# Kernel optimization log

Measured on AMD Instinct MI355X. Metric: run time of the kernel, lower is better.

The kernel has to match this reference:

```python
import jax, jax.numpy as jnp
import numpy as np
import math

H = 8        # n_heads
FACTOR = 5   # ProbSparse factor


def layer_norm(x, g, b, eps=1e-5):
    m = x.mean(-1, keepdims=True)
    v = ((x - m) ** 2).mean(-1, keepdims=True)
    return (x - m) / jnp.sqrt(v + eps) * g + b


def conv1d_circular(x, w, b=None):
    # x: [B, L, Cin], w: [Cout, Cin, 3]; Conv1d(k=3, padding=1, padding_mode='circular')
    xp = jnp.concatenate([x[:, -1:], x, x[:, :1]], axis=1)
    y = jax.lax.conv_general_dilated(xp.transpose(0, 2, 1), w, (1,), 'VALID',
                                     dimension_numbers=('NCH', 'OIH', 'NCH'))
    if b is not None:
        y = y + b[None, :, None]
    return y.transpose(0, 2, 1)


def pos_encoding(L, d):
    pos = jnp.arange(L, dtype=jnp.float32)[:, None]
    div = jnp.exp(jnp.arange(0, d, 2, dtype=jnp.float32) * (-math.log(10000.0) / d))
    pe = jnp.zeros((L, d), dtype=jnp.float32)
    pe = pe.at[:, 0::2].set(jnp.sin(pos * div))
    pe = pe.at[:, 1::2].set(jnp.cos(pos * div))
    return pe


def prob_attention(rng, Q, K, V):
    # Q, K, V: [B, H, L, E]; non-causal ProbSparse self-attention (mask_flag=False)
    B, Hh, L, E = Q.shape
    c = FACTOR * int(np.ceil(np.log(L)))
    U_part = min(c, L)  # sampled keys per query (sparsity measurement)
    u = min(c, L)       # number of active (top) queries
    idx = jax.random.randint(rng, (L, U_part), 0, L)          # shared over B,H as in torch
    K_sample = K[:, :, idx]                                   # [B,H,L,U,E] gather
    QK_sample = jnp.einsum('bhle,bhlue->bhlu', Q, K_sample)
    M = QK_sample.max(-1) - QK_sample.sum(-1) / L             # sparsity score per query
    M_top = jax.lax.top_k(M, u)[1]                            # [B,H,u] active query ids
    Q_red = jnp.take_along_axis(Q, M_top[..., None], axis=2)  # [B,H,u,E]
    scores = jnp.einsum('bhue,bhle->bhul', Q_red, K) * (1.0 / math.sqrt(E))
    attn = jax.nn.softmax(scores, axis=-1)
    upd = jnp.einsum('bhul,bhle->bhue', attn, V)
    # initial context: mean of V for every query; overwrite active queries
    ctx = jnp.broadcast_to(V.mean(axis=2, keepdims=True), (B, Hh, L, E))
    bi = jnp.arange(B)[:, None, None]
    hi = jnp.arange(Hh)[None, :, None]
    ctx = ctx.at[bi, hi, M_top].set(upd)
    return ctx.transpose(0, 2, 1, 3)  # [B,L,H,E]


def encoder_layer(rng, x, Wq, bq, Wk, bk, Wv, bv, Wo, bo, g1, b1, w1, bf1, w2, bf2, g2, b2):
    B, L, D = x.shape
    dh = D // H
    q = (x @ Wq.T + bq).reshape(B, L, H, dh).transpose(0, 2, 1, 3)
    k = (x @ Wk.T + bk).reshape(B, L, H, dh).transpose(0, 2, 1, 3)
    v = (x @ Wv.T + bv).reshape(B, L, H, dh).transpose(0, 2, 1, 3)
    o = prob_attention(rng, q, k, v).reshape(B, L, D)
    x = x + (o @ Wo.T + bo)            # dropout is identity in eval
    x = layer_norm(x, g1, b1)
    y = jax.nn.gelu(x @ w1.T + bf1, approximate=False)  # conv1 k=1 == linear
    y = y @ w2.T + bf2
    return layer_norm(x + y, g2, b2)


def conv_distill(x, w, b, bg, bb):
    # Conv1d(circular,k=3) -> BatchNorm1d(eval: mean 0, var 1) -> ELU -> MaxPool1d(3,2,1)
    y = conv1d_circular(x, w, b)
    y = y / math.sqrt(1.0 + 1e-5) * bg + bb
    y = jax.nn.elu(y)
    yc = jnp.pad(y.transpose(0, 2, 1), ((0, 0), (0, 0), (1, 1)), constant_values=-jnp.inf)
    p = jax.lax.reduce_window(yc, -jnp.inf, jax.lax.max, (1, 1, 3), (1, 1, 2), 'VALID')
    return p.transpose(0, 2, 1)  # [B, L//2, D]


def forward(x_enc, emb_w, Wq, bq, Wk, bk, Wv, bv, Wo, bo, ln1_g, ln1_b, ff_w1, ff_b1, ff_w2, ff_b2, ln2_g, ln2_b, cv_w, cv_b, bn_g, bn_b, norm_g, norm_b):
    B, L, _ = x_enc.shape
    D = emb_w.shape[0]
    x = conv1d_circular(x_enc, emb_w) + pos_encoding(L, D)[None]  # GazeEmbedding
    base = jax.random.key(42)
    EL = Wq.shape[0]
    for i in range(EL):
        rng = jax.random.fold_in(base, i)
        x = encoder_layer(rng, x, Wq[i], bq[i], Wk[i], bk[i], Wv[i], bv[i], Wo[i], bo[i],
                          ln1_g[i], ln1_b[i], ff_w1[i], ff_b1[i], ff_w2[i], ff_b2[i], ln2_g[i], ln2_b[i])
        if i < EL - 1:
            x = conv_distill(x, cv_w[i], cv_b[i], bn_g[i], bn_b[i])
    return layer_norm(x, norm_g, norm_b)


def setup_inputs() -> dict:
    key = jax.random.key(0)
    ks = jax.random.split(key, 16)
    B, L, C, D, F, EL = 4, 2048, 2, 512, 512, 3
    s = 0.02
    return {
        'x_enc': jax.random.normal(ks[0], (B, L, C), jnp.float32),
        'emb_w': jax.random.normal(ks[1], (D, C, 3), jnp.float32) * s,
        'Wq': jax.random.normal(ks[2], (EL, D, D), jnp.float32) * s,
        'bq': jnp.zeros((EL, D), jnp.float32),
        'Wk': jax.random.normal(ks[3], (EL, D, D), jnp.float32) * s,
        'bk': jnp.zeros((EL, D), jnp.float32),
        'Wv': jax.random.normal(ks[4], (EL, D, D), jnp.float32) * s,
        'bv': jnp.zeros((EL, D), jnp.float32),
        'Wo': jax.random.normal(ks[5], (EL, D, D), jnp.float32) * s,
        'bo': jnp.zeros((EL, D), jnp.float32),
        'ln1_g': jnp.ones((EL, D), jnp.float32),
        'ln1_b': jnp.zeros((EL, D), jnp.float32),
        'ff_w1': jax.random.normal(ks[6], (EL, F, D), jnp.float32) * s,
        'ff_b1': jnp.zeros((EL, F), jnp.float32),
        'ff_w2': jax.random.normal(ks[7], (EL, D, F), jnp.float32) * s,
        'ff_b2': jnp.zeros((EL, D), jnp.float32),
        'ln2_g': jnp.ones((EL, D), jnp.float32),
        'ln2_b': jnp.zeros((EL, D), jnp.float32),
        'cv_w': jax.random.normal(ks[8], (EL - 1, D, D, 3), jnp.float32) * s,
        'cv_b': jnp.zeros((EL - 1, D), jnp.float32),
        'bn_g': jnp.ones((EL - 1, D), jnp.float32),
        'bn_b': jnp.zeros((EL - 1, D), jnp.float32),
        'norm_g': jnp.ones((D,), jnp.float32),
        'norm_b': jnp.zeros((D,), jnp.float32),
    }


def reference(x_enc, emb_w, Wq, bq, Wk, bk, Wv, bv, Wo, bo, ln1_g, ln1_b, ff_w1, ff_b1, ff_w2, ff_b2, ln2_g, ln2_b, cv_w, cv_b, bn_g, bn_b, norm_g, norm_b):
    return forward(x_enc, emb_w, Wq, bq, Wk, bk, Wv, bv, Wo, bo, ln1_g, ln1_b, ff_w1, ff_b1, ff_w2, ff_b2, ln2_g, ln2_b, cv_w, cv_b, bn_g, bn_b, norm_g, norm_b)
```

## Files before the change

### kernel.cpp

```cpp
#include <hip/hip_runtime.h>
#include <cmath>
#include <cstdint>

#define D_MODEL 512
#define NH 8
#define DH 64

static inline int ceil_div(int a, int b) { return (a + b - 1) / b; }

typedef __attribute__((ext_vector_type(8))) short short8;
typedef __attribute__((ext_vector_type(4))) float floatx4;

__device__ __forceinline__ unsigned short f2bf(float f) {
  uint32_t u = __float_as_uint(f);
  uint32_t r = (u + 0x7fffu + ((u >> 16) & 1u)) >> 16;
  return (unsigned short)r;
}
__device__ __forceinline__ float bf2f(unsigned short s) {
  return __uint_as_float(((uint32_t)s) << 16);
}

#define TF_ROTL(x, r) (((x) << (r)) | ((x) >> (32 - (r))))

__host__ __device__ inline void threefry2x32(uint32_t k0, uint32_t k1,
                                             uint32_t x0, uint32_t x1,
                                             uint32_t* o0, uint32_t* o1) {
  uint32_t ks2 = k0 ^ k1 ^ 0x1BD11BDAu;
  x0 += k0; x1 += k1;
#define TF_R4(a, b, c, d)                                    \
  x0 += x1; x1 = TF_ROTL(x1, a); x1 ^= x0;                   \
  x0 += x1; x1 = TF_ROTL(x1, b); x1 ^= x0;                   \
  x0 += x1; x1 = TF_ROTL(x1, c); x1 ^= x0;                   \
  x0 += x1; x1 = TF_ROTL(x1, d); x1 ^= x0;
  TF_R4(13, 15, 26, 6);  x0 += k1;  x1 += ks2 + 1u;
  TF_R4(17, 29, 16, 24); x0 += ks2; x1 += k0 + 2u;
  TF_R4(13, 15, 26, 6);  x0 += k0;  x1 += k1 + 3u;
  TF_R4(17, 29, 16, 24); x0 += k1;  x1 += ks2 + 4u;
  TF_R4(13, 15, 26, 6);  x0 += ks2; x1 += k0 + 5u;
#undef TF_R4
  *o0 = x0; *o1 = x1;
}

__global__ __launch_bounds__(256) void cast3_qkv_kernel(
    const float* __restrict__ s0, const float* __restrict__ s1,
    const float* __restrict__ s2, unsigned short* __restrict__ dst) {
  int sel = blockIdx.x / 768, bb = blockIdx.x % 768;
  int i = (bb * 256 + threadIdx.x) * 4;
  const float* s = (sel == 0) ? s0 : (sel == 1) ? s1 : s2;
  float4 v = *(const float4*)(s + i);
  ushort4 o;
  o.x = f2bf(v.x); o.y = f2bf(v.y); o.z = f2bf(v.z); o.w = f2bf(v.w);
  int layer = i >> 18, off = i & 262143;
  *(ushort4*)(dst + (size_t)layer * 786432 + sel * 262144 + off) = o;
}

__global__ __launch_bounds__(256) void cast3_flat_kernel(
    const float* __restrict__ s0, const float* __restrict__ s1,
    const float* __restrict__ s2, unsigned short* __restrict__ dst) {
  int sel = blockIdx.x / 768, bb = blockIdx.x % 768;
  int i = (bb * 256 + threadIdx.x) * 4;
  const float* s = (sel == 0) ? s0 : (sel == 1) ? s1 : s2;
  float4 v = *(const float4*)(s + i);
  ushort4 o;
  o.x = f2bf(v.x); o.y = f2bf(v.y); o.z = f2bf(v.z); o.w = f2bf(v.w);
  *(ushort4*)(dst + (size_t)sel * 786432 + i) = o;
}

__global__ __launch_bounds__(256) void cast_cvperm_kernel(
    const float* __restrict__ src, unsigned short* __restrict__ dst) {
  int o = blockIdx.x * 256 + threadIdx.x;
  int m = o / 786432, rem = o % 786432;
  int n = rem / 1536, q = rem % 1536;
  int k = q >> 9, c = q & 511;
  dst[o] = f2bf(src[(size_t)m * 786432 + n * 1536 + c * 3 + k]);
}

__global__ __launch_bounds__(256) void embed_kernel(
    const float* __restrict__ x_enc, const float* __restrict__ emb_w,
    float* __restrict__ x, unsigned short* __restrict__ xb, int B, int L) {
  int i = blockIdx.x * 256 + threadIdx.x;
  int total = B * L * D_MODEL;
  if (i >= total) return;
  int d = i % D_MODEL;
  int l = (i / D_MODEL) % L;
  int b = i / (D_MODEL * L);
  int lm = (l == 0) ? (L - 1) : (l - 1);
  int lp = (l == L - 1) ? 0 : (l + 1);
  const float* w = emb_w + d * 6;
  const float* xb_in = x_enc + (size_t)b * L * 2;
  float acc = 0.f;
  acc += xb_in[lm * 2 + 0] * w[0] + xb_in[l * 2 + 0] * w[1] + xb_in[lp * 2 + 0] * w[2];
  acc += xb_in[lm * 2 + 1] * w[3] + xb_in[l * 2 + 1] * w[4] + xb_in[lp * 2 + 1] * w[5];
  int j = d >> 1;
  const float coef = -0.017988946039015985f;
  float div = expf((float)(2 * j) * coef);
  float ang = (float)l * div;
  float pe = (d & 1) ? cosf(ang) : sinf(ang);
  float v = acc + pe;
  x[i] = v;
  xb[i] = f2bf(v);
}

__global__ __launch_bounds__(256) void ln_kernel(
    const float* __restrict__ in, const float* __restrict__ g,
    const float* __restrict__ b, float* __restrict__ out) {
  int row = blockIdx.x;
  int t = threadIdx.x;
  const float* xr = in + (size_t)row * D_MODEL;
  float v0 = xr[t], v1 = xr[t + 256];
  __shared__ float red[256];
  red[t] = v0 + v1;
  __syncthreads();
  for (int s = 128; s > 0; s >>= 1) { if (t < s) red[t] += red[t + s]; __syncthreads(); }
  float mean = red[0] * (1.0f / 512.0f);
  __syncthreads();
  float d0 = v0 - mean, d1 = v1 - mean;
  red[t] = d0 * d0 + d1 * d1;
  __syncthreads();
  for (int s = 128; s > 0; s >>= 1) { if (t < s) red[t] += red[t + s]; __syncthreads(); }
  float var = red[0] * (1.0f / 512.0f);
  float rstd = 1.0f / sqrtf(var + 1e-5f);
  float* outr = out + (size_t)row * D_MODEL;
  outr[t]       = d0 * rstd * g[t]       + b[t];
  outr[t + 256] = d1 * rstd * g[t + 256] + b[t + 256];
}

__global__ __launch_bounds__(256) void ln_dual_kernel(
    const float* __restrict__ in, const float* __restrict__ g,
    const float* __restrict__ b, float* __restrict__ out,
    unsigned short* __restrict__ out16) {
  int row = blockIdx.x;
  int t = threadIdx.x;
  const float* xr = in + (size_t)row * D_MODEL;
  float v0 = xr[t], v1 = xr[t + 256];
  __shared__ float red[256];
  red[t] = v0 + v1;
  __syncthreads();
  for (int s = 128; s > 0; s >>= 1) { if (t < s) red[t] += red[t + s]; __syncthreads(); }
  float mean = red[0] * (1.0f / 512.0f);
  __syncthreads();
  float d0 = v0 - mean, d1 = v1 - mean;
  red[t] = d0 * d0 + d1 * d1;
  __syncthreads();
  for (int s = 128; s > 0; s >>= 1) { if (t < s) red[t] += red[t + s]; __syncthreads(); }
  float var = red[0] * (1.0f / 512.0f);
  float rstd = 1.0f / sqrtf(var + 1e-5f);
  float* outr = out + (size_t)row * D_MODEL;
  unsigned short* o16 = out16 + (size_t)row * D_MODEL;
  float r0 = d0 * rstd * g[t] + b[t];
  float r1 = d1 * rstd * g[t + 256] + b[t + 256];
  outr[t] = r0;       o16[t] = f2bf(r0);
  outr[t + 256] = r1; o16[t + 256] = f2bf(r1);
}

__device__ __forceinline__ float epilogue_apply(int MODE, float v, float r,
                                                float g, float bb, float scl) {
  if (MODE == 1) {
    v = 0.5f * v * (1.0f + erff(v * 0.7071067811865475f));
  } else if (MODE == 2) {
    v += r;
  } else if (MODE == 3) {
    v = v * scl * g + bb;
    v = (v > 0.f) ? v : expm1f(v);
  }
  return v;
}


__device__ __forceinline__ void gload16(const void* g, void* l) {
  __builtin_amdgcn_global_load_lds(
      (const __attribute__((address_space(1))) unsigned int*)g,
      (__attribute__((address_space(3))) unsigned int*)l, 16, 0, 0);
}

__device__ __forceinline__ int xcd_swz(int orig, int nwg) {
  int q = nwg >> 3, r = nwg & 7;
  int x = orig & 7, o = orig >> 3;
  return (x < r ? x * (q + 1) : r * (q + 1) + (x - r) * q) + o;
}

__device__ __forceinline__ void stage64(const unsigned short* __restrict__ G,
                                        int ldk, int row0, int k0,
                                        unsigned short* lds, int tid) {
  const int wave = tid >> 6;
#pragma unroll
  for (int iss = 0; iss < 2; ++iss) {
    int s = iss * 256 + tid;
    int r = s >> 3;
    int cs = (s & 7) ^ (r & 7);
    gload16(G + (size_t)(row0 + r) * ldk + k0 + cs * 8,
            lds + (size_t)(iss * 256 + wave * 64) * 8);
  }
}

__device__ __forceinline__ short8 frag64(const unsigned short* t, int row,
                                         int chunk) {
  return *(const short8*)(t + row * 64 + ((chunk ^ (row & 7)) * 8));
}

struct Acc4 { floatx4 v[2][2]; };

__device__ __forceinline__ void gemm64_core(
    const unsigned short* __restrict__ A, int lda,
    const unsigned short* __restrict__ Bt, int ldb, int K, int bm, int bn,
    unsigned short* lds , int tid, Acc4& out) {
  const int wave = tid >> 6, lane = tid & 63;
  const int wm = (wave >> 1) * 32, wn = (wave & 1) * 32;
  const int quad = lane >> 4, l16 = lane & 15;
  floatx4 z = {0.f, 0.f, 0.f, 0.f};
  floatx4 a00 = z, a01 = z, a10 = z, a11 = z;
  stage64(A, lda, bm, 0, lds, tid);
  stage64(Bt, ldb, bn, 0, lds + 4096, tid);
  __syncthreads();
  const int nk = K >> 6;
  for (int t = 0; t < nk; ++t) {
    const int cur = (t & 1) * 8192;
    if (t + 1 < nk) {
      const int nxt = 8192 - cur;
      stage64(A, lda, bm, (t + 1) << 6, lds + nxt, tid);
      stage64(Bt, ldb, bn, (t + 1) << 6, lds + nxt + 4096, tid);
    }
    const unsigned short* At = lds + cur;
    const unsigned short* Bl = lds + cur + 4096;
#pragma unroll
    for (int ks = 0; ks < 2; ++ks) {
      short8 f0 = frag64(At, wm + l16,      ks * 4 + quad);
      short8 f1 = frag64(At, wm + 16 + l16, ks * 4 + quad);
      short8 g0 = frag64(Bl, wn + l16,      ks * 4 + quad);
      short8 g1 = frag64(Bl, wn + 16 + l16, ks * 4 + quad);
      a00 = __builtin_amdgcn_mfma_f32_16x16x32_bf16(f0, g0, a00, 0, 0, 0);
      a01 = __builtin_amdgcn_mfma_f32_16x16x32_bf16(f0, g1, a01, 0, 0, 0);
      a10 = __builtin_amdgcn_mfma_f32_16x16x32_bf16(f1, g0, a10, 0, 0, 0);
      a11 = __builtin_amdgcn_mfma_f32_16x16x32_bf16(f1, g1, a11, 0, 0, 0);
    }
    __syncthreads();
  }
  out.v[0][0] = a00; out.v[0][1] = a01; out.v[1][0] = a10; out.v[1][1] = a11;
}

template <int MODE, int OUT>
__global__ __launch_bounds__(256) void bgemm_kernel(
    const unsigned short* __restrict__ A, const unsigned short* __restrict__ Bt,
    const float* __restrict__ bias, const float* __restrict__ R,
    const float* __restrict__ gvec, const float* __restrict__ bvec,
    float* __restrict__ C, unsigned short* __restrict__ C16,
    int M, int N, int K, float scl) {
  __shared__ unsigned short lds[16384];
  const int tid = threadIdx.x;
  const int gridN = N >> 6;
  const int wgid = xcd_swz(blockIdx.x, (int)gridDim.x);
  const int bn = (wgid % gridN) * 64;
  const int bm = (wgid / gridN) * 64;
  Acc4 acc;
  gemm64_core(A, K, Bt, K, K, bm, bn, lds, tid, acc);
  const int wave = tid >> 6, lane = tid & 63;
  const int wm = (wave >> 1) * 32, wn = (wave & 1) * 32;
  const int quad = lane >> 4, l16 = lane & 15;
#pragma unroll
  for (int i = 0; i < 2; ++i) {
#pragma unroll
    for (int j = 0; j < 2; ++j) {
      int col = bn + wn + j * 16 + l16;
#pragma unroll
      for (int p = 0; p < 4; ++p) {
        int row = bm + wm + i * 16 + quad * 4 + p;
        float v = acc.v[i][j][p] + bias[col];
        v = epilogue_apply(MODE, v, (MODE == 2) ? R[(size_t)row * N + col] : 0.f,
                           (MODE == 3) ? gvec[col] : 0.f,
                           (MODE == 3) ? bvec[col] : 0.f, scl);
        if (OUT & 1) C[(size_t)row * N + col] = v;
        if (OUT & 2) C16[(size_t)row * N + col] = f2bf(v);
      }
    }
  }
}

template <int MODE, int OUT>
static void run_bgemm(const unsigned short* A, const unsigned short* Bt,
                      const float* bias, const float* R, const float* g,
                      const float* bb, float* C, unsigned short* C16,
                      int M, int N, int K, float scl, hipStream_t stream) {
  int nwg = (N / 64) * (M / 64);
  bgemm_kernel<MODE, OUT><<<nwg, 256, 0, stream>>>(A, Bt, bias, R, g, bb, C,
                                                   C16, M, N, K, scl);
}

__global__ __launch_bounds__(256) void qkv_gemm_kernel(
    const unsigned short* __restrict__ A, const unsigned short* __restrict__ Bt,
    const float* __restrict__ bqp, const float* __restrict__ bkp,
    const float* __restrict__ bvp, float* __restrict__ Cq,
    float* __restrict__ Cv, unsigned short* __restrict__ K16o, int M, int K) {
  __shared__ unsigned short lds[16384];
  const int tid = threadIdx.x;
  const int gridN = 24;
  const int wgid = xcd_swz(blockIdx.x, (int)gridDim.x);
  const int bn = (wgid % gridN) * 64;
  const int bm = (wgid / gridN) * 64;
  Acc4 acc;
  gemm64_core(A, K, Bt, K, K, bm, bn, lds, tid, acc);
  const int wave = tid >> 6, lane = tid & 63;
  const int wm = (wave >> 1) * 32, wn = (wave & 1) * 32;
  const int quad = lane >> 4, l16 = lane & 15;
#pragma unroll
  for (int i = 0; i < 2; ++i) {
#pragma unroll
    for (int j = 0; j < 2; ++j) {
      int col = bn + wn + j * 16 + l16;
      int seg = col >> 9, nn = col & 511;
      const float* bp = (seg == 0) ? bqp : (seg == 1) ? bkp : bvp;
      float bsv = bp[nn];
#pragma unroll
      for (int p = 0; p < 4; ++p) {
        int row = bm + wm + i * 16 + quad * 4 + p;
        float v = acc.v[i][j][p] + bsv;
        if (seg == 1) {
          K16o[(size_t)row * 512 + nn] = f2bf(v);
        } else {
          float* Cd = (seg == 0) ? Cq : Cv;
          Cd[(size_t)row * 512 + nn] = v;
        }
      }
    }
  }
}

__global__ __launch_bounds__(256) void conv_gemm_kernel(
    const unsigned short* __restrict__ Axl, const unsigned short* __restrict__ Bt,
    const float* __restrict__ bias, const float* __restrict__ gvec,
    const float* __restrict__ bvec, float* __restrict__ C,
    int M, int L, int log2L, float scl) {
  __shared__ unsigned short lds[16384];
  const int tid = threadIdx.x;
  const int wgid = xcd_swz(blockIdx.x, (int)gridDim.x);
  const int bn = (wgid & 7) * 64;
  const int bm = (wgid >> 3) * 64;
  const int wave = tid >> 6, lane = tid & 63;
  const int wm = (wave >> 1) * 32, wn = (wave & 1) * 32;
  const int quad = lane >> 4, l16 = lane & 15;
  floatx4 z = {0.f, 0.f, 0.f, 0.f};
  floatx4 a00 = z, a01 = z, a10 = z, a11 = z;

#define STAGE_A_CONV(T, DST)                                               \
  {                                                                        \
    _Pragma("unroll") for (int iss = 0; iss < 2; ++iss) {                  \
      int s = iss * 256 + tid;                                             \
      int r = s >> 3;                                                      \
      int cs = (s & 7) ^ (r & 7);                                          \
      int row = bm + r;                                                    \
      int li = row & (L - 1);                                              \
      int bb2 = row >> log2L;                                              \
      int l2 = (li + ((T) >> 3) - 1 + L) & (L - 1);                        \
      gload16(Axl + (((size_t)((bb2 << log2L) + l2)) << 9) +               \
                  (((T) & 7) << 6) + cs * 8,                               \
              (DST) + (size_t)(iss * 256 + wave * 64) * 8);                \
    }                                                                      \
  }

  STAGE_A_CONV(0, lds);
  stage64(Bt, 1536, bn, 0, lds + 4096, tid);
  __syncthreads();
  for (int t = 0; t < 24; ++t) {
    const int cur = (t & 1) * 8192;
    if (t + 1 < 24) {
      const int nxt = 8192 - cur;
      STAGE_A_CONV(t + 1, lds + nxt);
      stage64(Bt, 1536, bn, (t + 1) << 6, lds + nxt + 4096, tid);
    }
    const unsigned short* At = lds + cur;
    const unsigned short* Bl = lds + cur + 4096;
#pragma unroll
    for (int ks = 0; ks < 2; ++ks) {
      short8 f0 = frag64(At, wm + l16,      ks * 4 + quad);
      short8 f1 = frag64(At, wm + 16 + l16, ks * 4 + quad);
      short8 g0 = frag64(Bl, wn + l16,      ks * 4 + quad);
      short8 g1 = frag64(Bl, wn + 16 + l16, ks * 4 + quad);
      a00 = __builtin_amdgcn_mfma_f32_16x16x32_bf16(f0, g0, a00, 0, 0, 0);
      a01 = __builtin_amdgcn_mfma_f32_16x16x32_bf16(f0, g1, a01, 0, 0, 0);
      a10 = __builtin_amdgcn_mfma_f32_16x16x32_bf16(f1, g0, a10, 0, 0, 0);
      a11 = __builtin_amdgcn_mfma_f32_16x16x32_bf16(f1, g1, a11, 0, 0, 0);
    }
    __syncthreads();
  }
#undef STAGE_A_CONV
  floatx4 accs[2][2] = {{a00, a01}, {a10, a11}};
#pragma unroll
  for (int i = 0; i < 2; ++i) {
#pragma unroll
    for (int j = 0; j < 2; ++j) {
      int col = bn + wn + j * 16 + l16;
      float gv = gvec[col], bbv = bvec[col], bsv = bias[col];
#pragma unroll
      for (int p = 0; p < 4; ++p) {
        int row = bm + wm + i * 16 + quad * 4 + p;
        float v = accs[i][j][p] + bsv;
        v = epilogue_apply(3, v, 0.f, gv, bbv, scl);
        C[(size_t)row * 512 + col] = v;
      }
    }
  }
}

__global__ __launch_bounds__(256) void sparse_qk_fused_kernel(
    const float* __restrict__ Q, const unsigned short* __restrict__ K16,
    float* __restrict__ Mout, int B, int L, int U, uint32_t k0, uint32_t k1) {
  __shared__ int idxl[64];
  __shared__ float wmax[4][8];
  __shared__ float wsum[4][8];
  int bl = blockIdx.x;
  int b = bl / L, l = bl - b * L;
  int tid = threadIdx.x;
  int wave = tid >> 6, lane = tid & 63;
  if (tid < U) {
    uint32_t o0, o1;
    threefry2x32(k0, k1, 0u, (uint32_t)(l * U + tid), &o0, &o1);
    idxl[tid] = (int)((o0 ^ o1) & (uint32_t)(L - 1));
  }
  int h = lane >> 3;
  const float4* qr = (const float4*)(Q + (size_t)bl * D_MODEL + lane * 8);
  float4 q0 = qr[0], q1 = qr[1];
  float qv[8] = {q0.x, q0.y, q0.z, q0.w, q1.x, q1.y, q1.z, q1.w};
  __syncthreads();
  float mx = -INFINITY, sm = 0.f;
  for (int u = wave; u < U; u += 4) {
    int ki = idxl[u];
    short8 k8 = *(const short8*)(K16 + ((size_t)b * L + ki) * D_MODEL + lane * 8);
    float p = 0.f;
#pragma unroll
    for (int e = 0; e < 8; ++e) p += qv[e] * bf2f((unsigned short)k8[e]);
    p += __shfl_xor(p, 1);
    p += __shfl_xor(p, 2);
    p += __shfl_xor(p, 4);
    mx = fmaxf(mx, p);
    sm += p;
  }
  if ((lane & 7) == 0) { wmax[wave][h] = mx; wsum[wave][h] = sm; }
  __syncthreads();
  if (tid < 8) {
    float m = fmaxf(fmaxf(wmax[0][tid], wmax[1][tid]),
                    fmaxf(wmax[2][tid], wmax[3][tid]));
    float s = wsum[0][tid] + wsum[1][tid] + wsum[2][tid] + wsum[3][tid];
    Mout[((size_t)(b * NH + tid)) * L + l] = m - s / (float)L;
  }
}

template <int NE>
__global__ __launch_bounds__(256) void topk_kernel(
    const float* __restrict__ Mv, const float* __restrict__ Q,
    int* __restrict__ Mtop, unsigned int* __restrict__ bmap,
    unsigned short* __restrict__ qred16, float* __restrict__ vmean,
    int words, int u, int L) {
  int bh = blockIdx.x;
  int b = bh >> 3, h = bh & 7;
  int t = threadIdx.x;
  int wave = t >> 6, lane = t & 63;
  const int base = wave * 64 * NE;
  const float* src = Mv + (size_t)bh * (NE * 256);
  uint32_t ov[NE];
#pragma unroll
  for (int i = 0; i < NE; ++i) {
    uint32_t bits = __float_as_uint(src[base + i * 64 + lane]);
    uint32_t m = (uint32_t)((int32_t)bits >> 31) | 0x80000000u;
    ov[i] = bits ^ m;
  }
  if (t < words) bmap[bh * words + t] = 0u;
  if (t < 64) vmean[bh * 64 + t] = 0.f;

  uint32_t T = 0;
  for (int bit = 31; bit >= 0; --bit) {
    uint32_t cand = T | (1u << bit);
    int c = 0;
#pragma unroll
    for (int i = 0; i < NE; ++i)
      c += (int)__popcll(__ballot(ov[i] >= cand));
    if (c >= u) T = cand;
  }
  int c_gt = 0;
#pragma unroll
  for (int i = 0; i < NE; ++i)
    c_gt += (int)__popcll(__ballot(ov[i] > T));
  int need = u - c_gt;
  int I = 0;
  for (int bit = 10; bit >= 0; --bit) {
    int cand = I | (1 << bit);
    int c = 0;
#pragma unroll
    for (int i = 0; i < NE; ++i)
      c += (int)__popcll(__ballot(ov[i] == T && (base + i * 64 + lane) < cand));
    if (c < need) I = cand;
  }
  __shared__ uint32_t kOrd[160];
  __shared__ int kIdx[160];
  __shared__ int smTop[40];
  int cnt_pre = 0;
#pragma unroll
  for (int i = 0; i < NE; ++i) {
    int ix = base + i * 64 + lane;
    bool sel = (ov[i] > T) || (ov[i] == T && ix <= I);
    unsigned long long bal = __ballot(sel);
    if (sel) {
      int pos = wave * u + cnt_pre +
                (int)__popcll(bal & ((1ull << lane) - 1ull));
      kOrd[pos] = ov[i];
      kIdx[pos] = ix;
    }
    cnt_pre += (int)__popcll(bal);
  }
  __syncthreads();
  int total = 4 * u;
  if (t < total) {
    uint32_t myo = kOrd[t];
    int myi = kIdx[t];
    int rank = 0;
    for (int j = 0; j < total; ++j) {
      uint32_t jo = kOrd[j];
      int ji = kIdx[j];
      rank += (jo > myo || (jo == myo && ji < myi)) ? 1 : 0;
    }
    if (rank < u) {
      Mtop[bh * u + rank] = myi;
      smTop[rank] = myi;
      atomicOr(&bmap[bh * words + (myi >> 5)], 1u << (myi & 31));
    }
  }
  __syncthreads();
  int d = t & 63;
  for (int r = t >> 6; r < 64; r += 4) {
    float v = 0.f;
    if (r < u) {
      int l = smTop[r];
      v = Q[((size_t)(b * L + l)) * D_MODEL + h * DH + d];
    }
    qred16[((size_t)bh * 64 + r) * 64 + d] = f2bf(v);
  }
}

static void run_topk(const float* Mv, const float* Q, int* Mtop,
                     unsigned int* bmap, unsigned short* qred16, float* vmean,
                     int L, int u, hipStream_t stream) {
  int words = L / 32;
  if (L == 2048)
    topk_kernel<8><<<32, 256, 0, stream>>>(Mv, Q, Mtop, bmap, qred16, vmean, words, u, L);
  else if (L == 1024)
    topk_kernel<4><<<32, 256, 0, stream>>>(Mv, Q, Mtop, bmap, qred16, vmean, words, u, L);
  else
    topk_kernel<2><<<32, 256, 0, stream>>>(Mv, Q, Mtop, bmap, qred16, vmean, words, u, L);
}

__global__ __launch_bounds__(256) void vmean_partial_kernel(
    const float* __restrict__ V, float* __restrict__ vmean, int L) {
  int b = blockIdx.y;
  int chunk = blockIdx.x;
  int rows = L >> 6;
  int t = threadIdx.x;
  const float* base = V + ((size_t)b * L + (size_t)chunk * rows) * D_MODEL;
  float s0 = 0.f, s1 = 0.f;
  for (int r = 0; r < rows; ++r) {
    s0 += base[(size_t)r * D_MODEL + t];
    s1 += base[(size_t)r * D_MODEL + t + 256];
  }
  float invL = 1.0f / (float)L;
  atomicAdd(&vmean[b * D_MODEL + t], s0 * invL);
  atomicAdd(&vmean[b * D_MODEL + t + 256], s1 * invL);
}

__global__ void fill_ctx_kernel(const float* __restrict__ vmean,
                                const unsigned int* __restrict__ bmap,
                                unsigned short* __restrict__ O16,
                                float* __restrict__ O32, int B, int L,
                                int words) {
  int i = blockIdx.x * 256 + threadIdx.x;
  int total = B * L * D_MODEL;
  if (i >= total) return;
  int dcol = i % D_MODEL;
  int l = (i / D_MODEL) % L;
  int b = i / (D_MODEL * L);
  int h = dcol >> 6;
  unsigned int w = bmap[(b * NH + h) * words + (l >> 5)];
  bool sel = (w >> (l & 31)) & 1u;
  O16[i] = f2bf(sel ? 0.f : vmean[b * D_MODEL + dcol]);
  if (sel) O32[i] = 0.f;
}

__global__ void cast_sel_kernel(const float* __restrict__ O32,
                                const int* __restrict__ Mtop,
                                unsigned short* __restrict__ O16, int L,
                                int U) {
  int z = blockIdx.x;
  int b = z >> 3, h = z & 7;
  int t = threadIdx.x;
  int d = t & 63;
  for (int r = t >> 6; r < U; r += 4) {
    int l = Mtop[z * U + r];
    size_t off = ((size_t)(b * L + l)) * D_MODEL + h * DH + d;
    O16[off] = f2bf(O32[off]);
  }
}

__global__ __launch_bounds__(256) void scores_mfma_kernel(
    const unsigned short* __restrict__ qred16,
    const unsigned short* __restrict__ k16, float* __restrict__ S, int L,
    int U) {
  __shared__ unsigned short lds[16384];
  const int z = blockIdx.y;
  const int b = z >> 3, h = z & 7;
  const int bn = blockIdx.x * 64;
  const int tid = threadIdx.x;
  Acc4 acc;
  gemm64_core(qred16 + (size_t)z * 4096, 64,
              k16 + (size_t)b * L * D_MODEL + h * DH, D_MODEL, 64, 0, bn, lds,
              tid, acc);
  float* Sz = S + (size_t)z * 64 * L;
  const int wave = tid >> 6, lane = tid & 63;
  const int wm = (wave >> 1) * 32, wn = (wave & 1) * 32;
  const int quad = lane >> 4, l16 = lane & 15;
#pragma unroll
  for (int i = 0; i < 2; ++i) {
#pragma unroll
    for (int j = 0; j < 2; ++j) {
      int col = bn + wn + j * 16 + l16;
#pragma unroll
      for (int p = 0; p < 4; ++p) {
        int row = wm + i * 16 + quad * 4 + p;
        if (row < U) Sz[(size_t)row * L + col] = 0.125f * acc.v[i][j][p];
      }
    }
  }
}

template <int LC>
__global__ __launch_bounds__(256) void softmax_stats_kernel(
    const float* __restrict__ S, float* __restrict__ mrow,
    float* __restrict__ lrow, int U) {
  constexpr int NE = LC / 256;
  int rid = blockIdx.x;
  int z = rid / U, r = rid % U;
  const float* row = S + (size_t)z * 64 * LC + (size_t)r * LC;
  int t = threadIdx.x;
  float vals[NE];
  float m = -INFINITY;
#pragma unroll
  for (int i = 0; i < NE; ++i) {
    vals[i] = row[t + i * 256];
    m = fmaxf(m, vals[i]);
  }
  __shared__ float red[256];
  red[t] = m;
  __syncthreads();
  for (int s = 128; s > 0; s >>= 1) { if (t < s) red[t] = fmaxf(red[t], red[t + s]); __syncthreads(); }
  m = red[0];
  __syncthreads();
  float sum = 0.f;
#pragma unroll
  for (int i = 0; i < NE; ++i) sum += expf(vals[i] - m);
  red[t] = sum;
  __syncthreads();
  for (int s = 128; s > 0; s >>= 1) { if (t < s) red[t] += red[t + s]; __syncthreads(); }
  if (t == 0) {
    mrow[z * 64 + r] = m;
    lrow[z * 64 + r] = 1.0f / red[0];
  }
}

static void run_stats(const float* S, float* mrow, float* lrow, int L, int U,
                      hipStream_t stream) {
  int blocks = 32 * U;
  if (L == 2048)      softmax_stats_kernel<2048><<<blocks, 256, 0, stream>>>(S, mrow, lrow, U);
  else if (L == 1024) softmax_stats_kernel<1024><<<blocks, 256, 0, stream>>>(S, mrow, lrow, U);
  else                softmax_stats_kernel<512><<<blocks, 256, 0, stream>>>(S, mrow, lrow, U);
}

#define PV_LC 128

template <int U>
__global__ __launch_bounds__(256) void pv_kernel(
    const float* __restrict__ P, const float* __restrict__ V,
    const float* __restrict__ mrow, const float* __restrict__ lrow,
    const int* __restrict__ Mtop, float* __restrict__ O, int L) {
  __shared__ float Pl[U][PV_LC];
  __shared__ float Vl[PV_LC][DH + 4];
  __shared__ float Msh[U], Ish[U];
  const int z = blockIdx.y;
  const int b = z / NH, h = z % NH;
  const int c0 = blockIdx.x * PV_LC;
  const int tid = threadIdx.x;
  if (tid < U) { Msh[tid] = mrow[z * 64 + tid]; Ish[tid] = lrow[z * 64 + tid]; }
  __syncthreads();
  const float* Pz = P + (size_t)z * 64 * L + c0;
  for (int i4 = tid; i4 < U * (PV_LC / 4); i4 += 256) {
    int r = i4 / (PV_LC / 4);
    int lq = (i4 % (PV_LC / 4)) * 4;
    float4 p4 = *(const float4*)(Pz + (size_t)r * L + lq);
    float mr = Msh[r], ir = Ish[r];
    Pl[r][lq + 0] = expf(p4.x - mr) * ir;
    Pl[r][lq + 1] = expf(p4.y - mr) * ir;
    Pl[r][lq + 2] = expf(p4.z - mr) * ir;
    Pl[r][lq + 3] = expf(p4.w - mr) * ir;
  }
  const float* Vb = V + ((size_t)b * L + c0) * D_MODEL + h * DH;
  for (int i4 = tid; i4 < PV_LC * (DH / 4); i4 += 256) {
    int l = i4 >> 4;
    int d4 = (i4 & 15) * 4;
    float4 v4 = *(const float4*)(Vb + (size_t)l * D_MODEL + d4);
    Vl[l][d4 + 0] = v4.x; Vl[l][d4 + 1] = v4.y;
    Vl[l][d4 + 2] = v4.z; Vl[l][d4 + 3] = v4.w;
  }
  __syncthreads();
  const int wave = tid >> 6, lane = tid & 63;
  constexpr int NJ = (U + 3) / 4;
  float acc[NJ] = {};
  for (int l = 0; l < PV_LC; ++l) {
    float vv = Vl[l][lane];
#pragma unroll
    for (int j = 0; j < NJ; ++j) {
      int r = wave + 4 * j;
      if (r < U) acc[j] += Pl[r][l] * vv;
    }
  }
#pragma unroll
  for (int j = 0; j < NJ; ++j) {
    int r = wave + 4 * j;
    if (r < U) {
      int ml = Mtop[z * U + r];
      atomicAdd(&O[((size_t)(b * L + ml)) * D_MODEL + h * DH + lane], acc[j]);
    }
  }
}

static void run_pv(const float* P, const float* V, const float* mrow,
                   const float* lrow, const int* Mtop, float* O, int L, int U,
                   hipStream_t stream) {
  dim3 gg(L / PV_LC, 32);
  if (U == 40)      pv_kernel<40><<<gg, 256, 0, stream>>>(P, V, mrow, lrow, Mtop, O, L);
  else if (U == 35) pv_kernel<35><<<gg, 256, 0, stream>>>(P, V, mrow, lrow, Mtop, O, L);
  else              pv_kernel<64><<<gg, 256, 0, stream>>>(P, V, mrow, lrow, Mtop, O, L);
}

__global__ void maxpool_kernel(const float* __restrict__ Y,
                               float* __restrict__ X,
                               unsigned short* __restrict__ Xb, int B, int L) {
  int Lo = L / 2;
  int i = blockIdx.x * 256 + threadIdx.x;
  int total = B * Lo * D_MODEL;
  if (i >= total) return;
  int d = i % D_MODEL;
  int lp = (i / D_MODEL) % Lo;
  int b = i / (D_MODEL * Lo);
  int l0 = 2 * lp - 1;
  float m = -INFINITY;
#pragma unroll
  for (int k = 0; k < 3; ++k) {
    int l = l0 + k;
    if (l >= 0 && l < L) m = fmaxf(m, Y[((size_t)(b * L + l)) * D_MODEL + d]);
  }
  X[i] = m;
  Xb[i] = f2bf(m);
}

extern "C" void kernel_launch(void* const* d_in, const int* in_sizes, int n_in,
                              void* d_out, int out_size, void* d_ws,
                              size_t ws_size, hipStream_t stream) {
  const float* x_enc  = (const float*)d_in[0];
  const float* emb_w  = (const float*)d_in[1];
  const float* Wq     = (const float*)d_in[2];
  const float* bq     = (const float*)d_in[3];
  const float* Wk     = (const float*)d_in[4];
  const float* bk     = (const float*)d_in[5];
  const float* Wv     = (const float*)d_in[6];
  const float* bv     = (const float*)d_in[7];
  const float* Wo     = (const float*)d_in[8];
  const float* bo     = (const float*)d_in[9];
  const float* ln1_g  = (const float*)d_in[10];
  const float* ln1_b  = (const float*)d_in[11];
  const float* ff_w1  = (const float*)d_in[12];
  const float* ff_b1  = (const float*)d_in[13];
  const float* ff_w2  = (const float*)d_in[14];
  const float* ff_b2  = (const float*)d_in[15];
  const float* ln2_g  = (const float*)d_in[16];
  const float* ln2_b  = (const float*)d_in[17];
  const float* cv_w   = (const float*)d_in[18];
  const float* cv_b   = (const float*)d_in[19];
  const float* bn_g   = (const float*)d_in[20];
  const float* bn_b   = (const float*)d_in[21];
  const float* norm_g = (const float*)d_in[22];
  const float* norm_b = (const float*)d_in[23];

  const int B = 4, L0 = 2048, EL = 3;
  const size_t SZ = (size_t)B * 2048 * 512;
  float* ws   = (float*)d_ws;
  float* xbuf = ws;
  float* ebuf = ws + SZ;
  float* qbuf = ws + 2 * SZ;
  float* kbuf = ws + 3 * SZ;
  float* vbuf = ws + 4 * SZ;
  float* obuf = ws + 5 * SZ;
  float* sm   = ws + 6 * SZ;
  float*         d_M     = sm;
  int*           d_Mtop  = (int*)(sm + 65536);
  float*         d_vmean = sm + 65536 + 1280;
  unsigned int*  d_bmap  = (unsigned int*)(sm + 65536 + 1280 + 2048);
  unsigned short* qred16 = (unsigned short*)(sm + 65536 + 1280 + 2048 + 2048);
  float*         d_mrow  = sm + 136448;
  float*         d_lrow  = sm + 138496;
  unsigned short* wgt  = (unsigned short*)(ws + 6 * SZ + 160000);
  unsigned short* qkvw = wgt;
  unsigned short* wof  = wgt + 3 * 786432;
  unsigned short* wow  = wof;
  unsigned short* w1w  = wof + 786432;
  unsigned short* w2w  = wof + 2 * 786432;
  unsigned short* cvw2 = wof + 3 * 786432;

  float* Sbuf = ebuf;
  const float inv_s = 1.0f / sqrtf(1.0f + 1e-5f);

  cast3_qkv_kernel<<<3 * 768, 256, 0, stream>>>(Wq, Wk, Wv, qkvw);
  cast3_flat_kernel<<<3 * 768, 256, 0, stream>>>(Wo, ff_w1, ff_w2, wof);
  cast_cvperm_kernel<<<6144, 256, 0, stream>>>(cv_w, cvw2);

  embed_kernel<<<ceil_div(B * L0 * D_MODEL, 256), 256, 0, stream>>>(
      x_enc, emb_w, xbuf, (unsigned short*)ebuf, B, L0);
  unsigned short* xb16 = (unsigned short*)ebuf;

  int L = L0;
  int log2L = 11;
  for (int i = 0; i < EL; ++i) {
    const int M_ = B * L;
    int c = 5 * (int)ceil(log((double)L));
    int U = c < L ? c : L;
    int words = L / 32;
    unsigned short* k16 = (unsigned short*)kbuf;

    qkv_gemm_kernel<<<24 * (M_ / 64), 256, 0, stream>>>(
        xb16, qkvw + (size_t)i * 786432, bq + i * 512, bk + i * 512,
        bv + i * 512, qbuf, vbuf, k16, M_, 512);

    uint32_t lk0, lk1, k20, k21;
    threefry2x32(0u, 42u, 0u, (uint32_t)i, &lk0, &lk1);
    threefry2x32(lk0, lk1, 0u, 1u, &k20, &k21);

    sparse_qk_fused_kernel<<<B * L, 256, 0, stream>>>(qbuf, k16, d_M, B, L, U,
                                                      k20, k21);
    run_topk(d_M, qbuf, d_Mtop, d_bmap, qred16, d_vmean, L, U, stream);
    vmean_partial_kernel<<<dim3(64, B), 256, 0, stream>>>(vbuf, d_vmean, L);
    unsigned short* ab16 = (unsigned short*)qbuf;
    fill_ctx_kernel<<<ceil_div(B * L * D_MODEL, 256), 256, 0, stream>>>(
        d_vmean, d_bmap, ab16, obuf, B, L, words);

    scores_mfma_kernel<<<dim3(L / 64, B * NH), 256, 0, stream>>>(qred16, k16,
                                                                 Sbuf, L, U);
    run_stats(Sbuf, d_mrow, d_lrow, L, U, stream);
    run_pv(Sbuf, vbuf, d_mrow, d_lrow, d_Mtop, obuf, L, U, stream);
    cast_sel_kernel<<<B * NH, 256, 0, stream>>>(obuf, d_Mtop, ab16, L, U);

    run_bgemm<2, 1>(ab16, wow + (size_t)i * 262144, bo + i * 512, xbuf,
                    nullptr, nullptr, ebuf, nullptr, M_, 512, 512, 0.f,
                    stream);
    ln_dual_kernel<<<M_, 256, 0, stream>>>(ebuf, ln1_g + i * 512,
                                           ln1_b + i * 512, xbuf, ab16);

    unsigned short* ff1b16 = (unsigned short*)obuf;
    run_bgemm<1, 2>(ab16, w1w + (size_t)i * 262144, ff_b1 + i * 512, nullptr,
                    nullptr, nullptr, nullptr, ff1b16, M_, 512, 512, 0.f,
                    stream);
    run_bgemm<2, 1>(ff1b16, w2w + (size_t)i * 262144, ff_b2 + i * 512, xbuf,
                    nullptr, nullptr, ebuf, nullptr, M_, 512, 512, 0.f,
                    stream);

    if (i < EL - 1) {
      unsigned short* xln16 = (unsigned short*)qbuf;
      ln_dual_kernel<<<M_, 256, 0, stream>>>(ebuf, ln2_g + i * 512,
                                             ln2_b + i * 512, xbuf, xln16);
      conv_gemm_kernel<<<8 * (M_ / 64), 256, 0, stream>>>(
          xln16, cvw2 + (size_t)i * 786432, cv_b + i * 512, bn_g + i * 512,
          bn_b + i * 512, ebuf, M_, L, log2L, inv_s);
      xb16 = (unsigned short*)vbuf + 6291456;
      maxpool_kernel<<<ceil_div(B * (L / 2) * D_MODEL, 256), 256, 0, stream>>>(
          ebuf, xbuf, xb16, B, L);
      L /= 2;
      log2L -= 1;
    } else {
      ln_kernel<<<M_, 256, 0, stream>>>(ebuf, ln2_g + i * 512,
                                        ln2_b + i * 512, xbuf);
    }
  }

  ln_kernel<<<B * L, 256, 0, stream>>>(xbuf, norm_g, norm_b, (float*)d_out);
}
```

Measured before the change: 708.4 us.

## Fuse softmax stats into PV, merge vmean into topk, drop selection bitmap

Softmax row statistics and the probability-times-V product now run in one kernel with one block per (batch, head), writing bf16 output directly. That removes the stats kernel, the fp32 output buffer, its atomics and the separate cast-back kernel. The V-mean reduction is folded into the top-k launch as extra blocks, and the vmean zeroing moves into the sparse QK kernel. The context fill is now bitmap-free and vectorised, since the PV kernel overwrites the selected rows afterwards. The trade-off is that the PV work drops to only 32 blocks that each loop serially over the full sequence, which sharply reduces parallelism on that stage.

```diff
diff --git a/kernel.cpp b/kernel.cpp
--- a/kernel.cpp
+++ b/kernel.cpp
@@ -402,7 +402,8 @@
 
 __global__ __launch_bounds__(256) void sparse_qk_fused_kernel(
     const float* __restrict__ Q, const unsigned short* __restrict__ K16,
-    float* __restrict__ Mout, int B, int L, int U, uint32_t k0, uint32_t k1) {
+    float* __restrict__ Mout, float* __restrict__ vmean, int B, int L, int U,
+    uint32_t k0, uint32_t k1) {
   __shared__ int idxl[64];
   __shared__ float wmax[4][8];
   __shared__ float wsum[4][8];
@@ -410,6 +411,9 @@
   int b = bl / L, l = bl - b * L;
   int tid = threadIdx.x;
   int wave = tid >> 6, lane = tid & 63;
+  if (bl == 0) {
+    for (int k2 = tid; k2 < 4 * D_MODEL; k2 += 256) vmean[k2] = 0.f;
+  }
   if (tid < U) {
     uint32_t o0, o1;
     threefry2x32(k0, k1, 0u, (uint32_t)(l * U + tid), &o0, &o1);
@@ -444,14 +448,30 @@
 }
 
 template <int NE>
-__global__ __launch_bounds__(256) void topk_kernel(
+__global__ __launch_bounds__(256) void topk_vmean_kernel(
     const float* __restrict__ Mv, const float* __restrict__ Q,
-    int* __restrict__ Mtop, unsigned int* __restrict__ bmap,
-    unsigned short* __restrict__ qred16, float* __restrict__ vmean,
-    int words, int u, int L) {
-  int bh = blockIdx.x;
+    const float* __restrict__ V, float* __restrict__ vmean,
+    int* __restrict__ Mtop, unsigned short* __restrict__ qred16,
+    int u, int L) {
+  int blk = blockIdx.x;
+  int t = threadIdx.x;
+  if (blk >= 32) {
+    int idx = blk - 32;
+    int b2 = idx >> 6, chunk = idx & 63;
+    int rows = L >> 6;
+    const float* base = V + ((size_t)b2 * L + (size_t)chunk * rows) * D_MODEL;
+    float s0 = 0.f, s1 = 0.f;
+    for (int r = 0; r < rows; ++r) {
+      s0 += base[(size_t)r * D_MODEL + t];
+      s1 += base[(size_t)r * D_MODEL + t + 256];
+    }
+    float invL = 1.0f / (float)L;
+    atomicAdd(&vmean[b2 * D_MODEL + t], s0 * invL);
+    atomicAdd(&vmean[b2 * D_MODEL + t + 256], s1 * invL);
+    return;
+  }
+  int bh = blk;
   int b = bh >> 3, h = bh & 7;
-  int t = threadIdx.x;
   int wave = t >> 6, lane = t & 63;
   const int base = wave * 64 * NE;
   const float* src = Mv + (size_t)bh * (NE * 256);
@@ -462,9 +482,6 @@
     uint32_t m = (uint32_t)((int32_t)bits >> 31) | 0x80000000u;
     ov[i] = bits ^ m;
   }
-  if (t < words) bmap[bh * words + t] = 0u;
-  if (t < 64) vmean[bh * 64 + t] = 0.f;
-
   uint32_t T = 0;
   for (int bit = 31; bit >= 0; --bit) {
     uint32_t cand = T | (1u << bit);
@@ -519,7 +536,6 @@
     if (rank < u) {
       Mtop[bh * u + rank] = myi;
       smTop[rank] = myi;
-      atomicOr(&bmap[bh * words + (myi >> 5)], 1u << (myi & 31));
     }
   }
   __syncthreads();
@@ -534,66 +550,30 @@
   }
 }
 
-static void run_topk(const float* Mv, const float* Q, int* Mtop,
-                     unsigned int* bmap, unsigned short* qred16, float* vmean,
-                     int L, int u, hipStream_t stream) {
-  int words = L / 32;
+static void run_topk(const float* Mv, const float* Q, const float* V,
+                     float* vmean, int* Mtop, unsigned short* qred16, int L,
+                     int u, int B, hipStream_t stream) {
+  int nblk = 32 + 64 * B;
   if (L == 2048)
-    topk_kernel<8><<<32, 256, 0, stream>>>(Mv, Q, Mtop, bmap, qred16, vmean, words, u, L);
+    topk_vmean_kernel<8><<<nblk, 256, 0, stream>>>(Mv, Q, V, vmean, Mtop, qred16, u, L);
   else if (L == 1024)
-    topk_kernel<4><<<32, 256, 0, stream>>>(Mv, Q, Mtop, bmap, qred16, vmean, words, u, L);
+    topk_vmean_kernel<4><<<nblk, 256, 0, stream>>>(Mv, Q, V, vmean, Mtop, qred16, u, L);
   else
-    topk_kernel<2><<<32, 256, 0, stream>>>(Mv, Q, Mtop, bmap, qred16, vmean, words, u, L);
-}
-
-__global__ __launch_bounds__(256) void vmean_partial_kernel(
-    const float* __restrict__ V, float* __restrict__ vmean, int L) {
-  int b = blockIdx.y;
-  int chunk = blockIdx.x;
-  int rows = L >> 6;
-  int t = threadIdx.x;
-  const float* base = V + ((size_t)b * L + (size_t)chunk * rows) * D_MODEL;
-  float s0 = 0.f, s1 = 0.f;
-  for (int r = 0; r < rows; ++r) {
-    s0 += base[(size_t)r * D_MODEL + t];
-    s1 += base[(size_t)r * D_MODEL + t + 256];
-  }
-  float invL = 1.0f / (float)L;
-  atomicAdd(&vmean[b * D_MODEL + t], s0 * invL);
-  atomicAdd(&vmean[b * D_MODEL + t + 256], s1 * invL);
-}
-
-__global__ void fill_ctx_kernel(const float* __restrict__ vmean,
-                                const unsigned int* __restrict__ bmap,
-                                unsigned short* __restrict__ O16,
-                                float* __restrict__ O32, int B, int L,
-                                int words) {
-  int i = blockIdx.x * 256 + threadIdx.x;
+    topk_vmean_kernel<2><<<nblk, 256, 0, stream>>>(Mv, Q, V, vmean, Mtop, qred16, u, L);
+}
+
+__global__ __launch_bounds__(256) void fill_ctx_kernel(
+    const float* __restrict__ vmean, unsigned short* __restrict__ O16, int B,
+    int L) {
+  int i4 = (blockIdx.x * 256 + threadIdx.x) * 4;
   int total = B * L * D_MODEL;
-  if (i >= total) return;
-  int dcol = i % D_MODEL;
-  int l = (i / D_MODEL) % L;
-  int b = i / (D_MODEL * L);
-  int h = dcol >> 6;
-  unsigned int w = bmap[(b * NH + h) * words + (l >> 5)];
-  bool sel = (w >> (l & 31)) & 1u;
-  O16[i] = f2bf(sel ? 0.f : vmean[b * D_MODEL + dcol]);
-  if (sel) O32[i] = 0.f;
-}
-
-__global__ void cast_sel_kernel(const float* __restrict__ O32,
-                                const int* __restrict__ Mtop,
-                                unsigned short* __restrict__ O16, int L,
-                                int U) {
-  int z = blockIdx.x;
-  int b = z >> 3, h = z & 7;
-  int t = threadIdx.x;
-  int d = t & 63;
-  for (int r = t >> 6; r < U; r += 4) {
-    int l = Mtop[z * U + r];
-    size_t off = ((size_t)(b * L + l)) * D_MODEL + h * DH + d;
-    O16[off] = f2bf(O32[off]);
-  }
+  if (i4 >= total) return;
+  int dcol = i4 & 511;
+  int b = i4 / (D_MODEL * L);
+  const float* vm = vmean + b * D_MODEL + dcol;
+  ushort4 o;
+  o.x = f2bf(vm[0]); o.y = f2bf(vm[1]); o.z = f2bf(vm[2]); o.w = f2bf(vm[3]);
+  *(ushort4*)(O16 + i4) = o;
 }
 
 __global__ __launch_bounds__(256) void scores_mfma_kernel(
@@ -627,112 +607,83 @@
   }
 }
 
-template <int LC>
-__global__ __launch_bounds__(256) void softmax_stats_kernel(
-    const float* __restrict__ S, float* __restrict__ mrow,
-    float* __restrict__ lrow, int U) {
-  constexpr int NE = LC / 256;
-  int rid = blockIdx.x;
-  int z = rid / U, r = rid % U;
-  const float* row = S + (size_t)z * 64 * LC + (size_t)r * LC;
-  int t = threadIdx.x;
-  float vals[NE];
-  float m = -INFINITY;
-#pragma unroll
-  for (int i = 0; i < NE; ++i) {
-    vals[i] = row[t + i * 256];
-    m = fmaxf(m, vals[i]);
-  }
-  __shared__ float red[256];
-  red[t] = m;
-  __syncthreads();
-  for (int s = 128; s > 0; s >>= 1) { if (t < s) red[t] = fmaxf(red[t], red[t + s]); __syncthreads(); }
-  m = red[0];
-  __syncthreads();
-  float sum = 0.f;
-#pragma unroll
-  for (int i = 0; i < NE; ++i) sum += expf(vals[i] - m);
-  red[t] = sum;
-  __syncthreads();
-  for (int s = 128; s > 0; s >>= 1) { if (t < s) red[t] += red[t + s]; __syncthreads(); }
-  if (t == 0) {
-    mrow[z * 64 + r] = m;
-    lrow[z * 64 + r] = 1.0f / red[0];
-  }
-}
-
-static void run_stats(const float* S, float* mrow, float* lrow, int L, int U,
-                      hipStream_t stream) {
-  int blocks = 32 * U;
-  if (L == 2048)      softmax_stats_kernel<2048><<<blocks, 256, 0, stream>>>(S, mrow, lrow, U);
-  else if (L == 1024) softmax_stats_kernel<1024><<<blocks, 256, 0, stream>>>(S, mrow, lrow, U);
-  else                softmax_stats_kernel<512><<<blocks, 256, 0, stream>>>(S, mrow, lrow, U);
-}
-
 #define PV_LC 128
 
 template <int U>
-__global__ __launch_bounds__(256) void pv_kernel(
-    const float* __restrict__ P, const float* __restrict__ V,
-    const float* __restrict__ mrow, const float* __restrict__ lrow,
-    const int* __restrict__ Mtop, float* __restrict__ O, int L) {
+__global__ __launch_bounds__(256) void attn_pv_kernel(
+    const float* __restrict__ S, const float* __restrict__ V,
+    const int* __restrict__ Mtop, unsigned short* __restrict__ O16, int L) {
   __shared__ float Pl[U][PV_LC];
   __shared__ float Vl[PV_LC][DH + 4];
   __shared__ float Msh[U], Ish[U];
-  const int z = blockIdx.y;
-  const int b = z / NH, h = z % NH;
-  const int c0 = blockIdx.x * PV_LC;
+  const int z = blockIdx.x;
+  const int b = z >> 3, h = z & 7;
   const int tid = threadIdx.x;
-  if (tid < U) { Msh[tid] = mrow[z * 64 + tid]; Ish[tid] = lrow[z * 64 + tid]; }
-  __syncthreads();
-  const float* Pz = P + (size_t)z * 64 * L + c0;
-  for (int i4 = tid; i4 < U * (PV_LC / 4); i4 += 256) {
-    int r = i4 / (PV_LC / 4);
-    int lq = (i4 % (PV_LC / 4)) * 4;
-    float4 p4 = *(const float4*)(Pz + (size_t)r * L + lq);
-    float mr = Msh[r], ir = Ish[r];
-    Pl[r][lq + 0] = expf(p4.x - mr) * ir;
-    Pl[r][lq + 1] = expf(p4.y - mr) * ir;
-    Pl[r][lq + 2] = expf(p4.z - mr) * ir;
-    Pl[r][lq + 3] = expf(p4.w - mr) * ir;
-  }
-  const float* Vb = V + ((size_t)b * L + c0) * D_MODEL + h * DH;
-  for (int i4 = tid; i4 < PV_LC * (DH / 4); i4 += 256) {
-    int l = i4 >> 4;
-    int d4 = (i4 & 15) * 4;
-    float4 v4 = *(const float4*)(Vb + (size_t)l * D_MODEL + d4);
-    Vl[l][d4 + 0] = v4.x; Vl[l][d4 + 1] = v4.y;
-    Vl[l][d4 + 2] = v4.z; Vl[l][d4 + 3] = v4.w;
-  }
-  __syncthreads();
   const int wave = tid >> 6, lane = tid & 63;
   constexpr int NJ = (U + 3) / 4;
+  const float* Sz = S + (size_t)z * 64 * L;
+  for (int j = 0; j < NJ; ++j) {
+    int r = wave + 4 * j;
+    if (r >= U) continue;
+    const float* row = Sz + (size_t)r * L;
+    float m = -INFINITY;
+    for (int c = lane; c < L; c += 64) m = fmaxf(m, row[c]);
+#pragma unroll
+    for (int k = 32; k; k >>= 1) m = fmaxf(m, __shfl_xor(m, k));
+    float s = 0.f;
+    for (int c = lane; c < L; c += 64) s += expf(row[c] - m);
+#pragma unroll
+    for (int k = 32; k; k >>= 1) s += __shfl_xor(s, k);
+    if (lane == 0) { Msh[r] = m; Ish[r] = 1.0f / s; }
+  }
+  __syncthreads();
   float acc[NJ] = {};
-  for (int l = 0; l < PV_LC; ++l) {
-    float vv = Vl[l][lane];
-#pragma unroll
-    for (int j = 0; j < NJ; ++j) {
-      int r = wave + 4 * j;
-      if (r < U) acc[j] += Pl[r][l] * vv;
-    }
+  for (int c0 = 0; c0 < L; c0 += PV_LC) {
+    for (int i4 = tid; i4 < U * (PV_LC / 4); i4 += 256) {
+      int r = i4 / (PV_LC / 4);
+      int lq = (i4 % (PV_LC / 4)) * 4;
+      float4 p4 = *(const float4*)(Sz + (size_t)r * L + c0 + lq);
+      float mr = Msh[r], ir = Ish[r];
+      Pl[r][lq + 0] = expf(p4.x - mr) * ir;
+      Pl[r][lq + 1] = expf(p4.y - mr) * ir;
+      Pl[r][lq + 2] = expf(p4.z - mr) * ir;
+      Pl[r][lq + 3] = expf(p4.w - mr) * ir;
+    }
+    const float* Vb = V + ((size_t)b * L + c0) * D_MODEL + h * DH;
+    for (int i4 = tid; i4 < PV_LC * (DH / 4); i4 += 256) {
+      int l = i4 >> 4;
+      int d4 = (i4 & 15) * 4;
+      float4 v4 = *(const float4*)(Vb + (size_t)l * D_MODEL + d4);
+      Vl[l][d4 + 0] = v4.x; Vl[l][d4 + 1] = v4.y;
+      Vl[l][d4 + 2] = v4.z; Vl[l][d4 + 3] = v4.w;
+    }
+    __syncthreads();
+    for (int l = 0; l < PV_LC; ++l) {
+      float vv = Vl[l][lane];
+#pragma unroll
+      for (int j = 0; j < NJ; ++j) {
+        int r = wave + 4 * j;
+        if (r < U) acc[j] += Pl[r][l] * vv;
+      }
+    }
+    __syncthreads();
   }
 #pragma unroll
   for (int j = 0; j < NJ; ++j) {
     int r = wave + 4 * j;
     if (r < U) {
       int ml = Mtop[z * U + r];
-      atomicAdd(&O[((size_t)(b * L + ml)) * D_MODEL + h * DH + lane], acc[j]);
-    }
-  }
-}
-
-static void run_pv(const float* P, const float* V, const float* mrow,
-                   const float* lrow, const int* Mtop, float* O, int L, int U,
-                   hipStream_t stream) {
-  dim3 gg(L / PV_LC, 32);
-  if (U == 40)      pv_kernel<40><<<gg, 256, 0, stream>>>(P, V, mrow, lrow, Mtop, O, L);
-  else if (U == 35) pv_kernel<35><<<gg, 256, 0, stream>>>(P, V, mrow, lrow, Mtop, O, L);
-  else              pv_kernel<64><<<gg, 256, 0, stream>>>(P, V, mrow, lrow, Mtop, O, L);
+      O16[((size_t)(b * L + ml)) * D_MODEL + h * DH + lane] = f2bf(acc[j]);
+    }
+  }
+}
+
+static void run_attn_pv(const float* S, const float* V, const int* Mtop,
+                        unsigned short* O16, int L, int U,
+                        hipStream_t stream) {
+  if (U == 40)      attn_pv_kernel<40><<<32, 256, 0, stream>>>(S, V, Mtop, O16, L);
+  else if (U == 35) attn_pv_kernel<35><<<32, 256, 0, stream>>>(S, V, Mtop, O16, L);
+  else              attn_pv_kernel<64><<<32, 256, 0, stream>>>(S, V, Mtop, O16, L);
 }
 
 __global__ void maxpool_kernel(const float* __restrict__ Y,
@@ -797,10 +748,7 @@
   float*         d_M     = sm;
   int*           d_Mtop  = (int*)(sm + 65536);
   float*         d_vmean = sm + 65536 + 1280;
-  unsigned int*  d_bmap  = (unsigned int*)(sm + 65536 + 1280 + 2048);
   unsigned short* qred16 = (unsigned short*)(sm + 65536 + 1280 + 2048 + 2048);
-  float*         d_mrow  = sm + 136448;
-  float*         d_lrow  = sm + 138496;
   unsigned short* wgt  = (unsigned short*)(ws + 6 * SZ + 160000);
   unsigned short* qkvw = wgt;
   unsigned short* wof  = wgt + 3 * 786432;
@@ -811,6 +759,7 @@
 
   float* Sbuf = ebuf;
   const float inv_s = 1.0f / sqrtf(1.0f + 1e-5f);
+  (void)obuf;
 
   cast3_qkv_kernel<<<3 * 768, 256, 0, stream>>>(Wq, Wk, Wv, qkvw);
   cast3_flat_kernel<<<3 * 768, 256, 0, stream>>>(Wo, ff_w1, ff_w2, wof);
@@ -826,7 +775,6 @@
     const int M_ = B * L;
     int c = 5 * (int)ceil(log((double)L));
     int U = c < L ? c : L;
-    int words = L / 32;
     unsigned short* k16 = (unsigned short*)kbuf;
 
     qkv_gemm_kernel<<<24 * (M_ / 64), 256, 0, stream>>>(
@@ -837,19 +785,16 @@
     threefry2x32(0u, 42u, 0u, (uint32_t)i, &lk0, &lk1);
     threefry2x32(lk0, lk1, 0u, 1u, &k20, &k21);
 
-    sparse_qk_fused_kernel<<<B * L, 256, 0, stream>>>(qbuf, k16, d_M, B, L, U,
-                                                      k20, k21);
-    run_topk(d_M, qbuf, d_Mtop, d_bmap, qred16, d_vmean, L, U, stream);
-    vmean_partial_kernel<<<dim3(64, B), 256, 0, stream>>>(vbuf, d_vmean, L);
+    sparse_qk_fused_kernel<<<B * L, 256, 0, stream>>>(qbuf, k16, d_M, d_vmean,
+                                                      B, L, U, k20, k21);
+    run_topk(d_M, qbuf, vbuf, d_vmean, d_Mtop, qred16, L, U, B, stream);
     unsigned short* ab16 = (unsigned short*)qbuf;
-    fill_ctx_kernel<<<ceil_div(B * L * D_MODEL, 256), 256, 0, stream>>>(
-        d_vmean, d_bmap, ab16, obuf, B, L, words);
+    fill_ctx_kernel<<<ceil_div(B * L * D_MODEL / 4, 256), 256, 0, stream>>>(
+        d_vmean, ab16, B, L);
 
     scores_mfma_kernel<<<dim3(L / 64, B * NH), 256, 0, stream>>>(qred16, k16,
                                                                  Sbuf, L, U);
-    run_stats(Sbuf, d_mrow, d_lrow, L, U, stream);
-    run_pv(Sbuf, vbuf, d_mrow, d_lrow, d_Mtop, obuf, L, U, stream);
-    cast_sel_kernel<<<B * NH, 256, 0, stream>>>(obuf, d_Mtop, ab16, L, U);
+    run_attn_pv(Sbuf, vbuf, d_Mtop, ab16, L, U, stream);
 
     run_bgemm<2, 1>(ab16, wow + (size_t)i * 262144, bo + i * 512, xbuf,
                     nullptr, nullptr, ebuf, nullptr, M_, 512, 512, 0.f,
```

Measured after the change: 1.406 ms. 98.5% more time.
